# Optimization experiments

Hardware: AMD Instinct MI355X
Metric: run time of the kernel (lower is better)

Reference implementation:

```python
import jax, jax.numpy as jnp
import numpy as np

ALPHA = 1.0
NEG = -1e20  # boundary value used by the torch module


def _compute_mu(W, alpha):
    """DTW location parameter mu: [B, Na+1, Nb+1].
    mu[i,j] = alpha*W[i-1,j-1] + logsumexp(mu[i-1,j], mu[i,j-1], mu[i-1,j-1]).
    Row-wise scan (outer over i) with an inner scan over j for the
    left-dependency; fully vectorized over batch.
    """
    B, Na, Nb = W.shape
    aW = alpha * W  # [B, Na, Nb]
    # row 0: mu[:,0,0]=0, mu[:,0,1:]=-1e20
    row0 = jnp.concatenate([jnp.zeros((B, 1), W.dtype),
                            jnp.full((B, Nb), NEG, W.dtype)], axis=1)

    def row_step(prev_row, w_row):  # prev_row [B, Nb+1], w_row [B, Nb]
        up = prev_row[:, 1:]    # mu[i-1, j]   for j=1..Nb -> [B, Nb]
        diag = prev_row[:, :-1]  # mu[i-1, j-1]            -> [B, Nb]

        def col_step(left, inp):
            u, d, w = inp  # each [B]
            val = w + jax.nn.logsumexp(jnp.stack([u, left, d], axis=0), axis=0)
            return val, val

        left0 = jnp.full((B,), NEG, W.dtype)  # mu[i, 0] = -1e20
        xs = (up.T, diag.T, w_row.T)          # scan over Nb
        _, vals = jax.lax.scan(col_step, left0, xs)  # [Nb, B]
        new_row = jnp.concatenate([jnp.full((B, 1), NEG, W.dtype), vals.T], axis=1)
        return new_row, new_row

    _, rows = jax.lax.scan(row_step, row0, jnp.swapaxes(aW, 0, 1))  # [Na, B, Nb+1]
    mu = jnp.concatenate([row0[:, None, :], jnp.swapaxes(rows, 0, 1)], axis=1)
    return mu  # [B, Na+1, Nb+1]


def _compute_pi(W, mu, mask, alpha):
    """Reduced transition tensor pi: [B, Na, Nb, 3] (softmax over moves)."""
    up = mu[:, :-1, 1:]    # mu[i-1, j]
    left = mu[:, 1:, :-1]  # mu[i, j-1]
    diag = mu[:, :-1, :-1]  # mu[i-1, j-1]
    raw = jnp.stack([up, left, diag], axis=-1) + alpha * W[..., None]
    return jax.nn.softmax(raw, axis=-1) * mask


def setup_inputs() -> dict:
    key = jax.random.key(0)
    k1, _ = jax.random.split(key)
    B, Na, Nb = 64, 384, 384
    W = jax.random.normal(k1, (B, Na, Nb), dtype=jnp.float32)
    mask = jnp.ones((B, Na, Nb, 1), dtype=jnp.float32)
    return {"W": W, "mask": mask}


def reference(W, mask):
    mu = _compute_mu(W, ALPHA)
    pi = _compute_pi(W, mu, mask, ALPHA)
    return (mu, pi)
```

## Files before the change

### kernel.cpp

```cpp
#include <hip/hip_runtime.h>

#define NA 384
#define NB 384
#define NBATCH 64
#define NEGV -1e20f
#define C 8
#define NCW 6
#define TOT_CH 56
#define LOG2E 1.44269504088896340736f
#define LN2   0.69314718055994530942f

typedef float f4 __attribute__((ext_vector_type(4)));
struct __attribute__((packed)) F3 { float x, y, z; };

struct SharedT {
    f4    stage[2][NCW][64 * 9];
    float wtile[NCW][512];
    float bound[NCW - 1][NB + 1];
    int   progress[NCW - 1];
    int   computed[NCW];
    int   drained[NCW][2];
};

__device__ __forceinline__ void loadW8(const float* __restrict__ Wb, int rbase,
                                       int kk, int l, float (&r)[8])
{
    const int rl = l >> 3, cc = l & 7;
    const int colb = 8 * kk + cc;
#pragma unroll
    for (int i = 0; i < 8; ++i) {
        const int row = 8 * i + rl;
        int col = colb - row;
        col = col < 0 ? 0 : (col > NB - 1 ? NB - 1 : col);
        r[i] = Wb[(size_t)(rbase + row) * NB + col];
    }
}

template<bool FULL>
__device__ __forceinline__ void chunk_body(
    int k, int w, int l, const float* __restrict__ Wb, int rbase,
    float (&wreg)[8], float& val, float& diag, SharedT& sh)
{
    const int s0 = 1 + k * C;
    f4* st = &sh.stage[k & 1][w][0];
    float* wt = &sh.wtile[w][0];

#pragma unroll
    for (int i = 0; i < 8; ++i) wt[i * 64 + l] = wreg[i];
    const int wb = (l >> 3) * 64 + ((l & 7) << 3);
    const f4 wlo = *(const f4*)(wt + wb);
    const f4 whi = *(const f4*)(wt + wb + 4);

    if (k + 1 < TOT_CH) loadW8(Wb, rbase, k + 1, l, wreg);

    if (k >= 2) {
        volatile int* dr = &sh.drained[w][k & 1];
        while (*dr < k - 2) __builtin_amdgcn_s_sleep(1);
        __builtin_amdgcn_sched_barrier(0);
        asm volatile("" ::: "memory");
    }

    if (w > 0 && s0 <= NB) {
        const int need = (s0 + C - 1 < NB) ? s0 + C - 1 : NB;
        volatile int* pr = &sh.progress[w - 1];
        while (*pr < need) { }
        __builtin_amdgcn_sched_barrier(0);
        asm volatile("" ::: "memory");
    }

    float bnd[C];
    if (w > 0) {
#pragma unroll
        for (int c = 0; c < C; ++c) {
            const int s = s0 + c;
            bnd[c] = sh.bound[w - 1][s <= NB ? s : NB];
        }
    }

    float wc[C];
    wc[0] = wlo.x * LOG2E; wc[1] = wlo.y * LOG2E;
    wc[2] = wlo.z * LOG2E; wc[3] = wlo.w * LOG2E;
    wc[4] = whi.x * LOG2E; wc[5] = whi.y * LOG2E;
    wc[6] = whi.z * LOG2E; wc[7] = whi.w * LOG2E;

    __builtin_amdgcn_s_setprio(1);
#pragma unroll
    for (int c = 0; c < C; ++c) {
        const int s = s0 + c;
        float upv = __int_as_float(__builtin_amdgcn_update_dpp(
            0, __float_as_int(val), 0x138 , 0xF, 0xF, false));
        if (l == 0) upv = (w > 0 && s <= NB) ? bnd[c] : NEGV;
        const int j = s - l;
        if (FULL || (j >= 1 && j <= NB)) {
            const float m  = fmaxf(fmaxf(upv, val), diag);
            const float eu = exp2f(upv  - m);
            const float el = exp2f(val  - m);
            const float ed = exp2f(diag - m);
            const float ssum = eu + el + ed;
            const float nv = wc[c] + m + __log2f(ssum);
            const float iv = __builtin_amdgcn_rcpf(ssum);
            f4 cell; cell.x = eu * iv; cell.y = el * iv; cell.z = ed * iv; cell.w = nv;
            st[l * 9 + c] = cell;
            if (w < NCW - 1 && l == 63) sh.bound[w][j] = nv;
            diag = upv;
            val  = nv;
        }
    }

    asm volatile("s_waitcnt lgkmcnt(0)" ::: "memory");
    if (l == 63) {
        if (w < NCW - 1) {
            const int done = s0 + C - 1 - 63;
            if (done >= 1) *(volatile int*)&sh.progress[w] = done;
        }
        *(volatile int*)&sh.computed[w] = k + 1;
    }
    __builtin_amdgcn_s_setprio(0);
}

__global__ __launch_bounds__(768, 1) void dtw_mu_pi(
    const float* __restrict__ W, const float* __restrict__ mask,
    float* __restrict__ mu, float* __restrict__ pi)
{
    __shared__ SharedT sh;

    const int b   = blockIdx.x;
    const int tid = threadIdx.x;
    const int w   = tid >> 6;
    const int l   = tid & 63;

    const float* Wb = W    + (size_t)b * NA * NB;
    const float* Mb = mask + (size_t)b * NA * NB;
    float* mub = mu + (size_t)b * (NA + 1) * (NB + 1);
    float* pib = pi + (size_t)b * NA * NB * 3;

    if (tid < 384) {
        mub[tid + 1] = NEGV;
        mub[(size_t)(tid + 1) * (NB + 1)] = NEGV;
    }
    if (tid == 0) mub[0] = 0.0f;
    if (tid < NCW - 1) sh.progress[tid] = 0;
    if (tid < NCW) sh.computed[tid] = 0;
    if (tid < 2 * NCW) sh.drained[tid >> 1][tid & 1] = -1;
    __syncthreads();

    if (w < NCW) {
        const int rbase = w << 6;
        float val  = NEGV;
        float diag = (rbase + l == 0) ? 0.0f : NEGV;
        float wreg[8];
        loadW8(Wb, rbase, 0, l, wreg);

        for (int k = 0; k < 8; ++k)
            chunk_body<false>(k, w, l, Wb, rbase, wreg, val, diag, sh);
        for (int k = 8; k < 48; ++k)
            chunk_body<true>(k, w, l, Wb, rbase, wreg, val, diag, sh);
        for (int k = 48; k < TOT_CH; ++k)
            chunk_body<false>(k, w, l, Wb, rbase, wreg, val, diag, sh);
    } else {
        const int cw    = w - NCW;
        const int rbase = cw << 6;

        auto issue_mask = [&](int k, float (&mk)[C]) {
            const int colbase = k * C;
#pragma unroll
            for (int q = 0; q < 8; ++q) {
                const int cell = q * 64 + l;
                const int lrow = cell >> 3;
                const int cc   = cell & 7;
                int col = colbase + cc - lrow;
                col = col < 0 ? 0 : (col >= NB ? NB - 1 : col);
                mk[q] = Mb[(size_t)(rbase + lrow) * NB + col];
            }
        };

        auto process = [&](auto FULLC, int k, float (&mk)[C]) {
            constexpr bool FULL = FULLC.value;
            volatile int* cp = &sh.computed[cw];
            while (*cp < k + 1) __builtin_amdgcn_s_sleep(1);
            __builtin_amdgcn_sched_barrier(0);
            asm volatile("" ::: "memory");

            const f4* st = &sh.stage[k & 1][cw][0];
            f4 v0, v1, v2, v3, v4, v5, v6, v7;
            {
                const int lr = l >> 3, cc = l & 7;
                v0 = st[lr * 9 + cc];
                v1 = st[(lr + 8)  * 9 + cc];
                v2 = st[(lr + 16) * 9 + cc];
                v3 = st[(lr + 24) * 9 + cc];
                v4 = st[(lr + 32) * 9 + cc];
                v5 = st[(lr + 40) * 9 + cc];
                v6 = st[(lr + 48) * 9 + cc];
                v7 = st[(lr + 56) * 9 + cc];
            }
            asm volatile("s_waitcnt lgkmcnt(0)" ::: "memory");
            if (l == 0) *(volatile int*)&sh.drained[cw][k & 1] = k;

            const int colbase = k * C;
            const f4 vv[8] = {v0, v1, v2, v3, v4, v5, v6, v7};
#pragma unroll
            for (int q = 0; q < 8; ++q) {
                const int cell = q * 64 + l;
                const int lrow = cell >> 3;
                const int cc   = cell & 7;
                const int col  = colbase + cc - lrow;
                if (FULL || (col >= 0 && col < NB)) {
                    const float m = mk[q];
                    const size_t g = ((size_t)(rbase + lrow) * NB + col) * 3;
                    F3 p3; p3.x = vv[q].x * m; p3.y = vv[q].y * m; p3.z = vv[q].z * m;
                    *(F3*)(pib + g) = p3;
                    mub[(size_t)(rbase + lrow + 1) * (NB + 1) + col + 1] = vv[q].w * LN2;
                }
            }
            if (k + 2 < TOT_CH) issue_mask(k + 2, mk);
        };

        float mkA[C], mkB[C];
        issue_mask(0, mkA);
        issue_mask(1, mkB);
        constexpr auto FT = std::integral_constant<bool, false>{};
        constexpr auto TT = std::integral_constant<bool, true>{};
        for (int k = 0; k < 8; k += 2) {
            process(FT, k, mkA); process(FT, k + 1, mkB);
        }
        for (int k = 8; k < 48; k += 2) {
            process(TT, k, mkA); process(TT, k + 1, mkB);
        }
        for (int k = 48; k < TOT_CH; k += 2) {
            process(FT, k, mkA); process(FT, k + 1, mkB);
        }
    }
}

extern "C" void kernel_launch(void* const* d_in, const int* in_sizes, int n_in,
                              void* d_out, int out_size, void* d_ws, size_t ws_size,
                              hipStream_t stream) {
    const float* W    = (const float*)d_in[0];
    const float* mask = (const float*)d_in[1];
    float* mu = (float*)d_out;
    float* pi = mu + (size_t)NBATCH * (NA + 1) * (NB + 1);

    hipLaunchKernelGGL(dtw_mu_pi, dim3(NBATCH), dim3(768), 0, stream,
                       W, mask, mu, pi);
}
```

Baseline: 173.7 us.

## Split pi into separate elementwise kernel and offload W staging to IO waves

The fused DTW kernel no longer computes softmax probabilities inside the serial wavefront. Only mu is stored to LDS, and the IO waves now prefetch W tiles into a double-buffered, padded LDS area guarded by a readiness flag. A second fully parallel kernel recomputes pi from mu, W and mask using exp(neighbor + w - mu), with vectorized loads and stores. This removes the rcp, multiplies, wide LDS stores and pi/mask traffic from the latency-bound recurrence. The cost is a second launch and rereading mu and W from global memory.

```diff
diff --git a/kernel.cpp b/kernel.cpp
--- a/kernel.cpp
+++ b/kernel.cpp
@@ -7,19 +7,20 @@
 #define C 8
 #define NCW 6
 #define TOT_CH 56
+#define WPITCH 68
 #define LOG2E 1.44269504088896340736f
 #define LN2   0.69314718055994530942f
 
 typedef float f4 __attribute__((ext_vector_type(4)));
-struct __attribute__((packed)) F3 { float x, y, z; };
-
-struct SharedT {
-    f4    stage[2][NCW][64 * 9];
-    float wtile[NCW][512];
+
+struct alignas(16) SharedT {
+    float stage[2][NCW][64 * 9];
+    float wtile[2][NCW][8 * WPITCH];
     float bound[NCW - 1][NB + 1];
     int   progress[NCW - 1];
     int   computed[NCW];
     int   drained[NCW][2];
+    int   wready[NCW];
 };
 
 __device__ __forceinline__ void loadW8(const float* __restrict__ Wb, int rbase,
@@ -37,21 +38,21 @@
 }
 
 template<bool FULL>
-__device__ __forceinline__ void chunk_body(
-    int k, int w, int l, const float* __restrict__ Wb, int rbase,
-    float (&wreg)[8], float& val, float& diag, SharedT& sh)
+__device__ __forceinline__ void chunk_body(int k, int w, int l,
+                                           float& val, float& diag, SharedT& sh)
 {
     const int s0 = 1 + k * C;
-    f4* st = &sh.stage[k & 1][w][0];
-    float* wt = &sh.wtile[w][0];
-
-#pragma unroll
-    for (int i = 0; i < 8; ++i) wt[i * 64 + l] = wreg[i];
-    const int wb = (l >> 3) * 64 + ((l & 7) << 3);
+
+    {
+        volatile int* wr = &sh.wready[w];
+        while (*wr < k + 1) { }
+        __builtin_amdgcn_sched_barrier(0);
+        asm volatile("" ::: "memory");
+    }
+    const float* wt = &sh.wtile[k & 1][w][0];
+    const int wb = (l >> 3) * WPITCH + (l & 7) * 8;
     const f4 wlo = *(const f4*)(wt + wb);
     const f4 whi = *(const f4*)(wt + wb + 4);
-
-    if (k + 1 < TOT_CH) loadW8(Wb, rbase, k + 1, l, wreg);
 
     if (k >= 2) {
         volatile int* dr = &sh.drained[w][k & 1];
@@ -59,7 +60,6 @@
         __builtin_amdgcn_sched_barrier(0);
         asm volatile("" ::: "memory");
     }
-
     if (w > 0 && s0 <= NB) {
         const int need = (s0 + C - 1 < NB) ? s0 + C - 1 : NB;
         volatile int* pr = &sh.progress[w - 1];
@@ -67,7 +67,6 @@
         __builtin_amdgcn_sched_barrier(0);
         asm volatile("" ::: "memory");
     }
-
     float bnd[C];
     if (w > 0) {
 #pragma unroll
@@ -76,13 +75,13 @@
             bnd[c] = sh.bound[w - 1][s <= NB ? s : NB];
         }
     }
-
     float wc[C];
     wc[0] = wlo.x * LOG2E; wc[1] = wlo.y * LOG2E;
     wc[2] = wlo.z * LOG2E; wc[3] = wlo.w * LOG2E;
     wc[4] = whi.x * LOG2E; wc[5] = whi.y * LOG2E;
     wc[6] = whi.z * LOG2E; wc[7] = whi.w * LOG2E;
 
+    float* st = &sh.stage[k & 1][w][0];
     __builtin_amdgcn_s_setprio(1);
 #pragma unroll
     for (int c = 0; c < C; ++c) {
@@ -96,17 +95,13 @@
             const float eu = exp2f(upv  - m);
             const float el = exp2f(val  - m);
             const float ed = exp2f(diag - m);
-            const float ssum = eu + el + ed;
-            const float nv = wc[c] + m + __log2f(ssum);
-            const float iv = __builtin_amdgcn_rcpf(ssum);
-            f4 cell; cell.x = eu * iv; cell.y = el * iv; cell.z = ed * iv; cell.w = nv;
-            st[l * 9 + c] = cell;
+            const float nv = wc[c] + m + __log2f(eu + el + ed);
+            st[l * 9 + c] = nv;
             if (w < NCW - 1 && l == 63) sh.bound[w][j] = nv;
             diag = upv;
             val  = nv;
         }
     }
-
     asm volatile("s_waitcnt lgkmcnt(0)" ::: "memory");
     if (l == 63) {
         if (w < NCW - 1) {
@@ -118,21 +113,54 @@
     __builtin_amdgcn_s_setprio(0);
 }
 
-__global__ __launch_bounds__(768, 1) void dtw_mu_pi(
-    const float* __restrict__ W, const float* __restrict__ mask,
-    float* __restrict__ mu, float* __restrict__ pi)
+template<bool FULL>
+__device__ __forceinline__ void io_iter(int k, int cw, int l,
+        const float* __restrict__ Wb, int rbase, float* __restrict__ mub,
+        SharedT& sh)
+{
+    float wreg[8];
+    const bool prep = (k + 2 < TOT_CH);
+    if (prep) loadW8(Wb, rbase, k + 2, l, wreg);
+
+    volatile int* cp = &sh.computed[cw];
+    while (*cp < k + 1) __builtin_amdgcn_s_sleep(1);
+    __builtin_amdgcn_sched_barrier(0);
+    asm volatile("" ::: "memory");
+
+    const float* st = &sh.stage[k & 1][cw][0];
+    float v[8];
+    const int lr = l >> 3, cc = l & 7;
+#pragma unroll
+    for (int q = 0; q < 8; ++q) v[q] = st[(lr + 8 * q) * 9 + cc];
+    asm volatile("s_waitcnt lgkmcnt(0)" ::: "memory");
+    if (l == 0) *(volatile int*)&sh.drained[cw][k & 1] = k;
+
+    if (prep) {
+        float* wt = &sh.wtile[k & 1][cw][0];
+#pragma unroll
+        for (int i = 0; i < 8; ++i) wt[i * WPITCH + l] = wreg[i];
+        asm volatile("s_waitcnt lgkmcnt(0)" ::: "memory");
+        if (l == 0) *(volatile int*)&sh.wready[cw] = k + 3;
+    }
+
+    const int colbase = k * C;
+#pragma unroll
+    for (int q = 0; q < 8; ++q) {
+        const int lrow = lr + 8 * q;
+        const int col  = colbase + cc - lrow;
+        if (FULL || (col >= 0 && col < NB))
+            mub[(size_t)(rbase + lrow + 1) * (NB + 1) + col + 1] = v[q] * LN2;
+    }
+}
+
+__global__ __launch_bounds__(768, 1) void dtw_mu(const float* __restrict__ W,
+                                                 float* __restrict__ mu)
 {
     __shared__ SharedT sh;
-
-    const int b   = blockIdx.x;
-    const int tid = threadIdx.x;
-    const int w   = tid >> 6;
-    const int l   = tid & 63;
-
-    const float* Wb = W    + (size_t)b * NA * NB;
-    const float* Mb = mask + (size_t)b * NA * NB;
+    const int b = blockIdx.x, tid = threadIdx.x;
+    const int w = tid >> 6, l = tid & 63;
+    const float* Wb = W + (size_t)b * NA * NB;
     float* mub = mu + (size_t)b * (NA + 1) * (NB + 1);
-    float* pib = pi + (size_t)b * NA * NB * 3;
 
     if (tid < 384) {
         mub[tid + 1] = NEGV;
@@ -140,7 +168,7 @@
     }
     if (tid == 0) mub[0] = 0.0f;
     if (tid < NCW - 1) sh.progress[tid] = 0;
-    if (tid < NCW) sh.computed[tid] = 0;
+    if (tid < NCW) { sh.computed[tid] = 0; sh.wready[tid] = 0; }
     if (tid < 2 * NCW) sh.drained[tid >> 1][tid & 1] = -1;
     __syncthreads();
 
@@ -148,89 +176,67 @@
         const int rbase = w << 6;
         float val  = NEGV;
         float diag = (rbase + l == 0) ? 0.0f : NEGV;
+        for (int k = 0; k < 8; ++k)       chunk_body<false>(k, w, l, val, diag, sh);
+        for (int k = 8; k < 48; ++k)      chunk_body<true >(k, w, l, val, diag, sh);
+        for (int k = 48; k < TOT_CH; ++k) chunk_body<false>(k, w, l, val, diag, sh);
+    } else {
+        const int cw = w - NCW, rbase = cw << 6;
         float wreg[8];
         loadW8(Wb, rbase, 0, l, wreg);
-
-        for (int k = 0; k < 8; ++k)
-            chunk_body<false>(k, w, l, Wb, rbase, wreg, val, diag, sh);
-        for (int k = 8; k < 48; ++k)
-            chunk_body<true>(k, w, l, Wb, rbase, wreg, val, diag, sh);
-        for (int k = 48; k < TOT_CH; ++k)
-            chunk_body<false>(k, w, l, Wb, rbase, wreg, val, diag, sh);
-    } else {
-        const int cw    = w - NCW;
-        const int rbase = cw << 6;
-
-        auto issue_mask = [&](int k, float (&mk)[C]) {
-            const int colbase = k * C;
-#pragma unroll
-            for (int q = 0; q < 8; ++q) {
-                const int cell = q * 64 + l;
-                const int lrow = cell >> 3;
-                const int cc   = cell & 7;
-                int col = colbase + cc - lrow;
-                col = col < 0 ? 0 : (col >= NB ? NB - 1 : col);
-                mk[q] = Mb[(size_t)(rbase + lrow) * NB + col];
-            }
-        };
-
-        auto process = [&](auto FULLC, int k, float (&mk)[C]) {
-            constexpr bool FULL = FULLC.value;
-            volatile int* cp = &sh.computed[cw];
-            while (*cp < k + 1) __builtin_amdgcn_s_sleep(1);
-            __builtin_amdgcn_sched_barrier(0);
-            asm volatile("" ::: "memory");
-
-            const f4* st = &sh.stage[k & 1][cw][0];
-            f4 v0, v1, v2, v3, v4, v5, v6, v7;
-            {
-                const int lr = l >> 3, cc = l & 7;
-                v0 = st[lr * 9 + cc];
-                v1 = st[(lr + 8)  * 9 + cc];
-                v2 = st[(lr + 16) * 9 + cc];
-                v3 = st[(lr + 24) * 9 + cc];
-                v4 = st[(lr + 32) * 9 + cc];
-                v5 = st[(lr + 40) * 9 + cc];
-                v6 = st[(lr + 48) * 9 + cc];
-                v7 = st[(lr + 56) * 9 + cc];
-            }
-            asm volatile("s_waitcnt lgkmcnt(0)" ::: "memory");
-            if (l == 0) *(volatile int*)&sh.drained[cw][k & 1] = k;
-
-            const int colbase = k * C;
-            const f4 vv[8] = {v0, v1, v2, v3, v4, v5, v6, v7};
-#pragma unroll
-            for (int q = 0; q < 8; ++q) {
-                const int cell = q * 64 + l;
-                const int lrow = cell >> 3;
-                const int cc   = cell & 7;
-                const int col  = colbase + cc - lrow;
-                if (FULL || (col >= 0 && col < NB)) {
-                    const float m = mk[q];
-                    const size_t g = ((size_t)(rbase + lrow) * NB + col) * 3;
-                    F3 p3; p3.x = vv[q].x * m; p3.y = vv[q].y * m; p3.z = vv[q].z * m;
-                    *(F3*)(pib + g) = p3;
-                    mub[(size_t)(rbase + lrow + 1) * (NB + 1) + col + 1] = vv[q].w * LN2;
-                }
-            }
-            if (k + 2 < TOT_CH) issue_mask(k + 2, mk);
-        };
-
-        float mkA[C], mkB[C];
-        issue_mask(0, mkA);
-        issue_mask(1, mkB);
-        constexpr auto FT = std::integral_constant<bool, false>{};
-        constexpr auto TT = std::integral_constant<bool, true>{};
-        for (int k = 0; k < 8; k += 2) {
-            process(FT, k, mkA); process(FT, k + 1, mkB);
-        }
-        for (int k = 8; k < 48; k += 2) {
-            process(TT, k, mkA); process(TT, k + 1, mkB);
-        }
-        for (int k = 48; k < TOT_CH; k += 2) {
-            process(FT, k, mkA); process(FT, k + 1, mkB);
-        }
-    }
+        {
+            float* wt = &sh.wtile[0][cw][0];
+#pragma unroll
+            for (int i = 0; i < 8; ++i) wt[i * WPITCH + l] = wreg[i];
+        }
+        loadW8(Wb, rbase, 1, l, wreg);
+        {
+            float* wt = &sh.wtile[1][cw][0];
+#pragma unroll
+            for (int i = 0; i < 8; ++i) wt[i * WPITCH + l] = wreg[i];
+        }
+        asm volatile("s_waitcnt lgkmcnt(0)" ::: "memory");
+        if (l == 0) *(volatile int*)&sh.wready[cw] = 2;
+
+        for (int k = 0; k < 8; ++k)       io_iter<false>(k, cw, l, Wb, rbase, mub, sh);
+        for (int k = 8; k < 48; ++k)      io_iter<true >(k, cw, l, Wb, rbase, mub, sh);
+        for (int k = 48; k < TOT_CH; ++k) io_iter<false>(k, cw, l, Wb, rbase, mub, sh);
+    }
+}
+
+__global__ __launch_bounds__(256) void dtw_pi(const float* __restrict__ W,
+        const float* __restrict__ mask, const float* __restrict__ mu,
+        float* __restrict__ pi)
+{
+    const long long idx = ((long long)blockIdx.x * 256 + threadIdx.x) * 4;
+    const int rr = (int)(idx / NB);
+    const int jj = (int)(idx - (long long)rr * NB);
+    const int b  = rr / NA;
+    const int ii = rr - b * NA;
+    const float* m0 = mu + (size_t)b * (NA + 1) * (NB + 1)
+                         + (size_t)ii * (NB + 1) + jj;
+    const float* m1 = m0 + (NB + 1);
+    const float d0 = m0[0], d1 = m0[1], d2 = m0[2], d3 = m0[3], d4 = m0[4];
+    const float L0 = m1[0], L1 = m1[1], L2 = m1[2], L3 = m1[3], L4 = m1[4];
+    const f4 wv = *(const f4*)(W + idx);
+    const f4 mk = *(const f4*)(mask + idx);
+
+    const float t0 = wv.x - L1, t1 = wv.y - L2, t2 = wv.z - L3, t3 = wv.w - L4;
+    f4 o0, o1, o2;
+    o0.x = exp2f((d1 + t0) * LOG2E) * mk.x;
+    o0.y = exp2f((L0 + t0) * LOG2E) * mk.x;
+    o0.z = exp2f((d0 + t0) * LOG2E) * mk.x;
+    o0.w = exp2f((d2 + t1) * LOG2E) * mk.y;
+    o1.x = exp2f((L1 + t1) * LOG2E) * mk.y;
+    o1.y = exp2f((d1 + t1) * LOG2E) * mk.y;
+    o1.z = exp2f((d3 + t2) * LOG2E) * mk.z;
+    o1.w = exp2f((L2 + t2) * LOG2E) * mk.z;
+    o2.x = exp2f((d2 + t2) * LOG2E) * mk.z;
+    o2.y = exp2f((d4 + t3) * LOG2E) * mk.w;
+    o2.z = exp2f((L3 + t3) * LOG2E) * mk.w;
+    o2.w = exp2f((d3 + t3) * LOG2E) * mk.w;
+
+    f4* po = (f4*)(pi + idx * 3);
+    po[0] = o0; po[1] = o1; po[2] = o2;
 }
 
 extern "C" void kernel_launch(void* const* d_in, const int* in_sizes, int n_in,
@@ -241,6 +247,10 @@
     float* mu = (float*)d_out;
     float* pi = mu + (size_t)NBATCH * (NA + 1) * (NB + 1);
 
-    hipLaunchKernelGGL(dtw_mu_pi, dim3(NBATCH), dim3(768), 0, stream,
+    hipLaunchKernelGGL(dtw_mu, dim3(NBATCH), dim3(768), 0, stream, W, mu);
+
+    const int cells  = NBATCH * NA * NB;
+    const int blocks = cells / (256 * 4);
+    hipLaunchKernelGGL(dtw_pi, dim3(blocks), dim3(256), 0, stream,
                        W, mask, mu, pi);
 }
```

Result: faster. 164.3 us (-5.4%).
